# Optimization experiments

Hardware: AMD Instinct MI355X
Metric: run time of the kernel (lower is better)

## Reference

```python
import jax, jax.numpy as jnp
import numpy as np

HIDDEN_DIM = 2048
NUM_HEADS = 16
HEAD_DIM = HIDDEN_DIM // NUM_HEADS


def setup_inputs() -> dict:
    key = jax.random.key(0)
    ks = jax.random.split(key, 5)
    B, S, D = 1, 4096, HIDDEN_DIM
    scale = 1.0 / np.sqrt(D)
    x = jax.random.normal(ks[0], (B, S, D), dtype=jnp.float32)
    w_q = jax.random.normal(ks[1], (D, D), dtype=jnp.float32) * scale
    w_k = jax.random.normal(ks[2], (D, D), dtype=jnp.float32) * scale
    w_v = jax.random.normal(ks[3], (D, D), dtype=jnp.float32) * scale
    w_o = jax.random.normal(ks[4], (D, D), dtype=jnp.float32) * scale
    return {"x": x, "w_q": w_q, "w_k": w_k, "w_v": w_v, "w_o": w_o, "causal": 1}


def reference(x, w_q, w_k, w_v, w_o, causal):
    B, S, D = x.shape
    H, Dh = NUM_HEADS, HEAD_DIM
    sm_scale = 1.0 / np.sqrt(Dh)

    # projections (x @ W.T)
    q = jnp.einsum('bsd,ed->bse', x, w_q).reshape(B, S, H, Dh).transpose(0, 2, 1, 3)
    k = jnp.einsum('bsd,ed->bse', x, w_k).reshape(B, S, H, Dh).transpose(0, 2, 1, 3)
    v = jnp.einsum('bsd,ed->bse', x, w_v).reshape(B, S, H, Dh).transpose(0, 2, 1, 3)

    # attention scores [B, H, S, S]; flash online-softmax == standard softmax
    scores = jnp.einsum('bhqd,bhkd->bhqk', q, k) * sm_scale
    if causal:
        qpos = jnp.arange(S)[:, None]
        kpos = jnp.arange(S)[None, :]
        scores = jnp.where(qpos >= kpos, scores, -jnp.inf)
    probs = jax.nn.softmax(scores, axis=-1)
    o = jnp.einsum('bhqk,bhkd->bhqd', probs, v)  # [B, H, S, Dh]
    o = o.transpose(0, 2, 1, 3).reshape(B, S, D)
    return jnp.einsum('bsd,ed->bse', o, w_o)
```

## Files before the change

### kernel.cpp

```cpp
#include <hip/hip_runtime.h>
#include <stdint.h>

typedef __bf16 bf16_t;
typedef __bf16 bf16x8 __attribute__((ext_vector_type(8)));
typedef __bf16 bf16x4 __attribute__((ext_vector_type(4)));
typedef float  f32x4  __attribute__((ext_vector_type(4)));

static constexpr int S  = 4096;
static constexpr int D  = 2048;
static constexpr int H  = 16;
static constexpr int DH = 128;

__device__ __forceinline__ bf16x8 ld8(const bf16_t* p) { return *(const bf16x8*)p; }
__device__ __forceinline__ bf16x8 ld8c(const float* p) {
  const f32x4 a = *(const f32x4*)p;
  const f32x4 b = *(const f32x4*)(p + 4);
  bf16x8 r;
  r[0] = (bf16_t)a[0]; r[1] = (bf16_t)a[1]; r[2] = (bf16_t)a[2]; r[3] = (bf16_t)a[3];
  r[4] = (bf16_t)b[0]; r[5] = (bf16_t)b[1]; r[6] = (bf16_t)b[2]; r[7] = (bf16_t)b[3];
  return r;
}

__device__ __forceinline__ void async_ld16(const bf16_t* g, bf16_t* lds) {
  __builtin_amdgcn_global_load_lds(
      (const __attribute__((address_space(1))) uint32_t*)g,
      (__attribute__((address_space(3))) uint32_t*)lds, 16, 0, 0);
}

__global__ __launch_bounds__(256) void cvt_kernel(
    const float* __restrict__ x,  const float* __restrict__ wq,
    const float* __restrict__ wk, const float* __restrict__ wv,
    const float* __restrict__ wo,
    bf16_t* __restrict__ xb,  bf16_t* __restrict__ wqb,
    bf16_t* __restrict__ wkb, bf16_t* __restrict__ wvb,
    bf16_t* __restrict__ wob) {
  const int z = blockIdx.z;
  const float* src; bf16_t* dst; size_t off = 0;
  if      (z == 0) { src = x;  dst = xb;  off = 0; }
  else if (z == 1) { src = x;  dst = xb;  off = 4194304; }
  else if (z == 2) { src = wq; dst = wqb; }
  else if (z == 3) { src = wk; dst = wkb; }
  else if (z == 4) { src = wv; dst = wvb; }
  else             { src = wo; dst = wob; }
  const size_t i = off + ((size_t)blockIdx.x * 256 + threadIdx.x) * 8;
  *(bf16x8*)(dst + i) = ld8c(src + i);
}

template <typename TC, bool TR>
__device__ __forceinline__ void gemm_async(const bf16_t* __restrict__ A,
                                           const bf16_t* __restrict__ W,
                                           TC* __restrict__ C) {
  constexpr int K  = D;
  constexpr int BK = 32;
  __shared__ __align__(16) bf16_t Ash[128 * BK];
  __shared__ __align__(16) bf16_t Bsh[128 * BK];
  const int tid = threadIdx.x;
  const int w = tid >> 6, lane = tid & 63;
  const int c = lane & 15, g = lane >> 4;
  const int wm = w >> 1, wn = w & 1;
  const int rowBase = blockIdx.y * 128;
  const int colBase = blockIdx.x * 128;

  f32x4 acc[4][4] = {};

  for (int k0 = 0; k0 < K; k0 += BK) {
    __syncthreads();
    #pragma unroll
    for (int r = 0; r < 2; ++r) {
      const int cid = r * 256 + tid;
      const int row = cid >> 2, q = cid & 3;
      async_ld16(A + (size_t)(rowBase + row) * K + k0 + q * 8,
                 Ash + r * 2048 + w * 512);
      async_ld16(W + (size_t)(colBase + row) * K + k0 + q * 8,
                 Bsh + r * 2048 + w * 512);
    }
    __syncthreads();

    bf16x8 af[4], bf[4];
    #pragma unroll
    for (int i = 0; i < 4; ++i) af[i] = ld8(Ash + (wm * 64 + i * 16 + c) * BK + g * 8);
    #pragma unroll
    for (int j = 0; j < 4; ++j) bf[j] = ld8(Bsh + (wn * 64 + j * 16 + c) * BK + g * 8);
    #pragma unroll
    for (int i = 0; i < 4; ++i)
      #pragma unroll
      for (int j = 0; j < 4; ++j)
        acc[i][j] = __builtin_amdgcn_mfma_f32_16x16x32_bf16(af[i], bf[j], acc[i][j], 0, 0, 0);
  }

  #pragma unroll
  for (int i = 0; i < 4; ++i)
    #pragma unroll
    for (int j = 0; j < 4; ++j) {
      if (TR) {
        const int col  = colBase + wn * 64 + j * 16 + c;
        const int row0 = rowBase + wm * 64 + i * 16 + g * 4;
        bf16x4 v;
        #pragma unroll
        for (int r = 0; r < 4; ++r) v[r] = (bf16_t)acc[i][j][r];
        *(bf16x4*)((bf16_t*)C + (size_t)col * S + row0) = v;
      } else {
        #pragma unroll
        for (int r = 0; r < 4; ++r) {
          const int row = rowBase + wm * 64 + i * 16 + g * 4 + r;
          const int col = colBase + wn * 64 + j * 16 + c;
          C[(size_t)row * D + col] = (TC)acc[i][j][r];
        }
      }
    }
}

__global__ __launch_bounds__(256) void qkv_gemm_bf16(
    const bf16_t* __restrict__ X,
    const bf16_t* __restrict__ Wq, const bf16_t* __restrict__ Wk,
    const bf16_t* __restrict__ Wv,
    bf16_t* __restrict__ Qo, bf16_t* __restrict__ Ko, bf16_t* __restrict__ VTo) {
  if (blockIdx.z == 0)      gemm_async<bf16_t, false>(X, Wq, Qo);
  else if (blockIdx.z == 1) gemm_async<bf16_t, false>(X, Wk, Ko);
  else                      gemm_async<bf16_t, true >(X, Wv, VTo);
}

__global__ __launch_bounds__(256) void out_gemm_bf16(
    const bf16_t* __restrict__ A, const bf16_t* __restrict__ W,
    float* __restrict__ C) {
  gemm_async<float, false>(A, W, C);
}

__global__ __launch_bounds__(512, 2) void attn_kernel(
    const bf16_t* __restrict__ Q, const bf16_t* __restrict__ Kb,
    const bf16_t* __restrict__ VTg, bf16_t* __restrict__ O,
    const int* __restrict__ causal_p) {
  __shared__ __align__(16) bf16_t smem[40960];
  bf16_t* const KB0 = smem;
  bf16_t* const VB0 = smem + 16384;
  bf16_t* const Psh = smem + 32768;

  const int tid = threadIdx.x, w = tid >> 6, lane = tid & 63;
  const int c = lane & 15, g = lane >> 4;
  const int wq = w >> 1, wk = w & 1;
  const int causal = causal_p[0];
  constexpr float QS = 0.08838834764831845f * 1.4426950408889634f;

  const int bx = blockIdx.x;
  const int jj = bx >> 4;
  const int t = causal ? ((jj < 16) ? (31 - jj) : (jj - 16)) : jj;
  const int h = bx & 15;
  const int wrow = t * 128 + wq * 32;
  const int ktiles = causal ? (2 * t + 2) : (S / 64);

  int knA[2], qK8[2], dVA[2], qV8[2];
  #pragma unroll
  for (int r = 0; r < 2; ++r) {
    const int cid = r * 512 + tid;
    knA[r] = cid >> 4; qK8[r] = (((cid & 15) ^ (knA[r] & 7)) << 3);
    dVA[r] = cid >> 3; qV8[r] = (((cid & 7) ^ (dVA[r] & 7)) << 3);
  }

  bf16_t* const Pw = Psh + w * 1024;

  bf16x8 qf[2][4];
  #pragma unroll
  for (int i = 0; i < 2; ++i)
    #pragma unroll
    for (int kf = 0; kf < 4; ++kf) {
      const bf16x8 raw = ld8(Q + (size_t)(wrow + i * 16 + c) * D + h * DH + kf * 32 + g * 8);
      bf16x8 sc;
      #pragma unroll
      for (int e = 0; e < 8; ++e) sc[e] = (bf16_t)((float)raw[e] * QS);
      qf[i][kf] = sc;
    }

  f32x4 o_acc[2][8] = {};
  f32x4 psum[2] = {};

  #pragma unroll
  for (int r = 0; r < 2; ++r) {
    async_ld16(Kb + (size_t)knA[r] * D + h * DH + qK8[r], KB0 + r * 4096 + w * 512);
    async_ld16(VTg + (size_t)(h * DH + dVA[r]) * S + qV8[r], VB0 + r * 4096 + w * 512);
  }
  __syncthreads();

  int cur = 0;
  for (int kt = 0; kt < ktiles; ++kt) {
    if (kt + 1 < ktiles) {
      const int alt = cur ^ 1;
      #pragma unroll
      for (int r = 0; r < 2; ++r) {
        async_ld16(Kb + (size_t)((kt + 1) * 64 + knA[r]) * D + h * DH + qK8[r],
                   KB0 + alt * 8192 + r * 4096 + w * 512);
        async_ld16(VTg + (size_t)(h * DH + dVA[r]) * S + (kt + 1) * 64 + qV8[r],
                   VB0 + alt * 8192 + r * 4096 + w * 512);
      }
    }

    const bf16_t* const KB = KB0 + cur * 8192;
    const bf16_t* const VB = VB0 + cur * 8192;

    const bool active = !causal || (kt * 64 + wk * 32 <= wrow + 31);
    if (active) {
      __builtin_amdgcn_s_setprio(1);
      #pragma unroll
      for (int nf = 0; nf < 2; ++nf) {
        const int rr = wk * 32 + nf * 16 + c;
        f32x4 s[2] = {};
        #pragma unroll
        for (int kf = 0; kf < 4; ++kf) {
          const bf16x8 kk = ld8(KB + rr * 128 + ((((kf << 2) + g) ^ (rr & 7)) << 3));
          s[0] = __builtin_amdgcn_mfma_f32_16x16x32_bf16(qf[0][kf], kk, s[0], 0, 0, 0);
          s[1] = __builtin_amdgcn_mfma_f32_16x16x32_bf16(qf[1][kf], kk, s[1], 0, 0, 0);
        }
        if (causal && (kt * 64 + wk * 32 + nf * 16 + 15 > wrow)) {
          #pragma unroll
          for (int i = 0; i < 2; ++i)
            #pragma unroll
            for (int r_ = 0; r_ < 4; ++r_) {
              const int kc2 = kt * 64 + wk * 32 + nf * 16 + c;
              const int qr = wrow + i * 16 + g * 4 + r_;
              if (kc2 > qr) s[i][r_] = -1e30f;
            }
        }
        #pragma unroll
        for (int i = 0; i < 2; ++i)
          #pragma unroll
          for (int r_ = 0; r_ < 4; ++r_) {
            const int qrl = i * 16 + g * 4 + r_;
            const float pv = exp2f(s[i][r_]);
            psum[i][r_] += pv;
            const int ch = (((nf << 1) + (c >> 3)) + (qrl >> 1)) & 3;
            Pw[qrl * 32 + (ch << 3) + (c & 7)] = (bf16_t)pv;
          }
      }

      bf16x8 pf[2];
      #pragma unroll
      for (int i = 0; i < 2; ++i) {
        const int rowp = i * 16 + c;
        pf[i] = ld8(Pw + rowp * 32 + (((g + (rowp >> 1)) & 3) << 3));
      }
      #pragma unroll
      for (int nf = 0; nf < 8; ++nf) {
        const int dl = nf * 16 + c;
        const bf16x8 vf = ld8(VB + dl * 64 + ((((wk << 2) + g) ^ (dl & 7)) << 3));
        o_acc[0][nf] = __builtin_amdgcn_mfma_f32_16x16x32_bf16(pf[0], vf, o_acc[0][nf], 0, 0, 0);
        o_acc[1][nf] = __builtin_amdgcn_mfma_f32_16x16x32_bf16(pf[1], vf, o_acc[1][nf], 0, 0, 0);
      }
      __builtin_amdgcn_s_setprio(0);
    }

    __syncthreads();
    cur ^= 1;
  }

  float* const scr = (float*)smem;
  float* const slot = scr + (size_t)(wq * 64 + lane) * 72;
  if (wk == 1) {
    #pragma unroll
    for (int i = 0; i < 2; ++i) {
      #pragma unroll
      for (int nf = 0; nf < 8; ++nf)
        *(f32x4*)(slot + (i * 8 + nf) * 4) = o_acc[i][nf];
      *(f32x4*)(slot + 64 + i * 4) = psum[i];
    }
  }
  __syncthreads();
  if (wk == 0) {
    #pragma unroll
    for (int i = 0; i < 2; ++i) {
      #pragma unroll
      for (int nf = 0; nf < 8; ++nf)
        o_acc[i][nf] += *(const f32x4*)(slot + (i * 8 + nf) * 4);
      psum[i] += *(const f32x4*)(slot + 64 + i * 4);
    }
    #pragma unroll
    for (int i = 0; i < 2; ++i)
      #pragma unroll
      for (int r_ = 0; r_ < 4; ++r_) {
        float v = psum[i][r_];
        v += __shfl_xor(v, 1); v += __shfl_xor(v, 2);
        v += __shfl_xor(v, 4); v += __shfl_xor(v, 8);
        const float inv = 1.0f / v;
        const int row = wrow + i * 16 + g * 4 + r_;
        #pragma unroll
        for (int nf = 0; nf < 8; ++nf)
          O[(size_t)row * D + h * DH + nf * 16 + c] = (bf16_t)(o_acc[i][nf][r_] * inv);
      }
  }
}

extern "C" void kernel_launch(void* const* d_in, const int* in_sizes, int n_in,
                              void* d_out, int out_size, void* d_ws, size_t ws_size,
                              hipStream_t stream) {
  const float* x  = (const float*)d_in[0];
  const float* wq = (const float*)d_in[1];
  const float* wk = (const float*)d_in[2];
  const float* wv = (const float*)d_in[3];
  const float* wo = (const float*)d_in[4];
  const int* causal = (const int*)d_in[5];
  float* out = (float*)d_out;

  bf16_t* Qb  = (bf16_t*)d_ws;
  bf16_t* Kb  = Qb + (size_t)S * D;
  bf16_t* VTb = Kb + (size_t)S * D;
  bf16_t* Ob  = VTb + (size_t)S * D;
  bf16_t* xb  = Ob + (size_t)S * D;
  bf16_t* wqb = xb + (size_t)S * D;
  bf16_t* wkb = wqb + (size_t)D * D;
  bf16_t* wvb = wkb + (size_t)D * D;
  bf16_t* wob = wvb + (size_t)D * D;

  dim3 blk(256);
  cvt_kernel<<<dim3(2048, 1, 6), blk, 0, stream>>>(x, wq, wk, wv, wo,
                                                   xb, wqb, wkb, wvb, wob);
  qkv_gemm_bf16<<<dim3(D / 128, S / 128, 3), blk, 0, stream>>>(xb, wqb, wkb, wvb,
                                                               Qb, Kb, VTb);
  attn_kernel<<<dim3(512), dim3(512), 0, stream>>>(Qb, Kb, VTb, Ob, causal);
  out_gemm_bf16<<<dim3(D / 128, S / 128), blk, 0, stream>>>(Ob, wob, out);
}
```

Before: 442.6 us.

## Use persistent attention blocks with atomic work queue over 64-row query tiles

The attention kernel becomes persistent. Each block takes work items (head, 64-row query tile) from a global atomic counter, ordered longest-first under causal masking, instead of one fixed 128-row tile per block. Each wave now covers 16 query rows, computes S transposed (K as the A operand), and writes P as packed bf16x4 into a smaller LDS buffer. The aim is better load balance across CUs under the causal triangle. The cost is twice as many K/V tile loads per query row and an extra memset plus atomic synchronisation per item.

```diff
diff --git a/kernel.cpp b/kernel.cpp
--- a/kernel.cpp
+++ b/kernel.cpp
@@ -129,24 +129,18 @@
 __global__ __launch_bounds__(512, 2) void attn_kernel(
     const bf16_t* __restrict__ Q, const bf16_t* __restrict__ Kb,
     const bf16_t* __restrict__ VTg, bf16_t* __restrict__ O,
-    const int* __restrict__ causal_p) {
-  __shared__ __align__(16) bf16_t smem[40960];
+    const int* __restrict__ causal_p, int* __restrict__ ctr) {
+  __shared__ __align__(16) bf16_t smem[36864];
   bf16_t* const KB0 = smem;
   bf16_t* const VB0 = smem + 16384;
   bf16_t* const Psh = smem + 32768;
+  __shared__ int item_s;
 
   const int tid = threadIdx.x, w = tid >> 6, lane = tid & 63;
   const int c = lane & 15, g = lane >> 4;
   const int wq = w >> 1, wk = w & 1;
   const int causal = causal_p[0];
   constexpr float QS = 0.08838834764831845f * 1.4426950408889634f;
-
-  const int bx = blockIdx.x;
-  const int jj = bx >> 4;
-  const int t = causal ? ((jj < 16) ? (31 - jj) : (jj - 16)) : jj;
-  const int h = bx & 15;
-  const int wrow = t * 128 + wq * 32;
-  const int ktiles = causal ? (2 * t + 2) : (S / 64);
 
   int knA[2], qK8[2], dVA[2], qV8[2];
   #pragma unroll
@@ -156,134 +150,122 @@
     dVA[r] = cid >> 3; qV8[r] = (((cid & 7) ^ (dVA[r] & 7)) << 3);
   }
 
-  bf16_t* const Pw = Psh + w * 1024;
-
-  bf16x8 qf[2][4];
-  #pragma unroll
-  for (int i = 0; i < 2; ++i)
+  bf16_t* const Pw = Psh + w * 512;
+  const int psw = (c >> 1) & 3;
+
+  while (true) {
+    __syncthreads();
+    if (tid == 0) item_s = atomicAdd(ctr, 1);
+    __syncthreads();
+    const int it = item_s;
+    if (it >= 1024) break;
+    const int s64 = causal ? (63 - (it >> 4)) : (it >> 4);
+    const int h = it & 15;
+    const int qrow0 = s64 * 64 + wq * 16;
+    const int ktiles = causal ? (s64 + 1) : (S / 64);
+
+    bf16x8 qf[4];
     #pragma unroll
     for (int kf = 0; kf < 4; ++kf) {
-      const bf16x8 raw = ld8(Q + (size_t)(wrow + i * 16 + c) * D + h * DH + kf * 32 + g * 8);
+      const bf16x8 raw = ld8(Q + (size_t)(qrow0 + c) * D + h * DH + kf * 32 + g * 8);
       bf16x8 sc;
       #pragma unroll
       for (int e = 0; e < 8; ++e) sc[e] = (bf16_t)((float)raw[e] * QS);
-      qf[i][kf] = sc;
-    }
-
-  f32x4 o_acc[2][8] = {};
-  f32x4 psum[2] = {};
-
-  #pragma unroll
-  for (int r = 0; r < 2; ++r) {
-    async_ld16(Kb + (size_t)knA[r] * D + h * DH + qK8[r], KB0 + r * 4096 + w * 512);
-    async_ld16(VTg + (size_t)(h * DH + dVA[r]) * S + qV8[r], VB0 + r * 4096 + w * 512);
-  }
-  __syncthreads();
-
-  int cur = 0;
-  for (int kt = 0; kt < ktiles; ++kt) {
-    if (kt + 1 < ktiles) {
-      const int alt = cur ^ 1;
-      #pragma unroll
-      for (int r = 0; r < 2; ++r) {
-        async_ld16(Kb + (size_t)((kt + 1) * 64 + knA[r]) * D + h * DH + qK8[r],
-                   KB0 + alt * 8192 + r * 4096 + w * 512);
-        async_ld16(VTg + (size_t)(h * DH + dVA[r]) * S + (kt + 1) * 64 + qV8[r],
-                   VB0 + alt * 8192 + r * 4096 + w * 512);
+      qf[kf] = sc;
+    }
+
+    f32x4 o_acc[8] = {};
+    float psum = 0.0f;
+
+    #pragma unroll
+    for (int r = 0; r < 2; ++r) {
+      async_ld16(Kb + (size_t)knA[r] * D + h * DH + qK8[r], KB0 + r * 4096 + w * 512);
+      async_ld16(VTg + (size_t)(h * DH + dVA[r]) * S + qV8[r], VB0 + r * 4096 + w * 512);
+    }
+    __syncthreads();
+
+    int cur = 0;
+    for (int kt = 0; kt < ktiles; ++kt) {
+      if (kt + 1 < ktiles) {
+        const int alt = cur ^ 1;
+        #pragma unroll
+        for (int r = 0; r < 2; ++r) {
+          async_ld16(Kb + (size_t)((kt + 1) * 64 + knA[r]) * D + h * DH + qK8[r],
+                     KB0 + alt * 8192 + r * 4096 + w * 512);
+          async_ld16(VTg + (size_t)(h * DH + dVA[r]) * S + (kt + 1) * 64 + qV8[r],
+                     VB0 + alt * 8192 + r * 4096 + w * 512);
+        }
       }
-    }
-
-    const bf16_t* const KB = KB0 + cur * 8192;
-    const bf16_t* const VB = VB0 + cur * 8192;
-
-    const bool active = !causal || (kt * 64 + wk * 32 <= wrow + 31);
-    if (active) {
-      __builtin_amdgcn_s_setprio(1);
-      #pragma unroll
-      for (int nf = 0; nf < 2; ++nf) {
-        const int rr = wk * 32 + nf * 16 + c;
-        f32x4 s[2] = {};
-        #pragma unroll
-        for (int kf = 0; kf < 4; ++kf) {
-          const bf16x8 kk = ld8(KB + rr * 128 + ((((kf << 2) + g) ^ (rr & 7)) << 3));
-          s[0] = __builtin_amdgcn_mfma_f32_16x16x32_bf16(qf[0][kf], kk, s[0], 0, 0, 0);
-          s[1] = __builtin_amdgcn_mfma_f32_16x16x32_bf16(qf[1][kf], kk, s[1], 0, 0, 0);
-        }
-        if (causal && (kt * 64 + wk * 32 + nf * 16 + 15 > wrow)) {
+
+      const bf16_t* const KB = KB0 + cur * 8192;
+      const bf16_t* const VB = VB0 + cur * 8192;
+      const int kb = kt * 64 + wk * 32;
+
+      const bool active = !causal || (kb <= qrow0 + 15);
+      if (active) {
+        __builtin_amdgcn_s_setprio(1);
+        #pragma unroll
+        for (int nf = 0; nf < 2; ++nf) {
+          const int rr = wk * 32 + nf * 16 + c;
+          f32x4 s = {};
           #pragma unroll
-          for (int i = 0; i < 2; ++i)
+          for (int kf = 0; kf < 4; ++kf) {
+            const bf16x8 kk = ld8(KB + rr * 128 + ((((kf << 2) + g) ^ (rr & 7)) << 3));
+            s = __builtin_amdgcn_mfma_f32_16x16x32_bf16(kk, qf[kf], s, 0, 0, 0);
+          }
+          if (causal && (kb + nf * 16 + 15 > qrow0)) {
             #pragma unroll
-            for (int r_ = 0; r_ < 4; ++r_) {
-              const int kc2 = kt * 64 + wk * 32 + nf * 16 + c;
-              const int qr = wrow + i * 16 + g * 4 + r_;
-              if (kc2 > qr) s[i][r_] = -1e30f;
-            }
-        }
-        #pragma unroll
-        for (int i = 0; i < 2; ++i)
+            for (int r_ = 0; r_ < 4; ++r_)
+              if (kb + nf * 16 + g * 4 + r_ > qrow0 + c) s[r_] = -1e30f;
+          }
+          bf16x4 pq;
           #pragma unroll
           for (int r_ = 0; r_ < 4; ++r_) {
-            const int qrl = i * 16 + g * 4 + r_;
-            const float pv = exp2f(s[i][r_]);
-            psum[i][r_] += pv;
-            const int ch = (((nf << 1) + (c >> 3)) + (qrl >> 1)) & 3;
-            Pw[qrl * 32 + (ch << 3) + (c & 7)] = (bf16_t)pv;
+            const float pv = exp2f(s[r_]);
+            psum += pv;
+            pq[r_] = (bf16_t)pv;
           }
+          const int p  = (nf << 1) | (g >> 1);
+          const int pp = ((p ^ psw) << 1) | (g & 1);
+          *(bf16x4*)(Pw + c * 32 + pp * 4) = pq;
+        }
+
+        const bf16x8 pf = ld8(Pw + c * 32 + ((g ^ psw) << 3));
+        #pragma unroll
+        for (int nf = 0; nf < 8; ++nf) {
+          const int dl = nf * 16 + c;
+          const bf16x8 vf = ld8(VB + dl * 64 + ((((wk << 2) + g) ^ (dl & 7)) << 3));
+          o_acc[nf] = __builtin_amdgcn_mfma_f32_16x16x32_bf16(pf, vf, o_acc[nf], 0, 0, 0);
+        }
+        __builtin_amdgcn_s_setprio(0);
       }
 
-      bf16x8 pf[2];
-      #pragma unroll
-      for (int i = 0; i < 2; ++i) {
-        const int rowp = i * 16 + c;
-        pf[i] = ld8(Pw + rowp * 32 + (((g + (rowp >> 1)) & 3) << 3));
+      __syncthreads();
+      cur ^= 1;
+    }
+
+    float* const slot = (float*)smem + (size_t)(wq * 64 + lane) * 36;
+    if (wk == 1) {
+      #pragma unroll
+      for (int nf = 0; nf < 8; ++nf) *(f32x4*)(slot + nf * 4) = o_acc[nf];
+      slot[32] = psum;
+    }
+    __syncthreads();
+    if (wk == 0) {
+      #pragma unroll
+      for (int nf = 0; nf < 8; ++nf) o_acc[nf] += *(const f32x4*)(slot + nf * 4);
+      psum += slot[32];
+      float v = psum;
+      v += __shfl_xor(v, 16); v += __shfl_xor(v, 32);
+      #pragma unroll
+      for (int r_ = 0; r_ < 4; ++r_) {
+        const float inv = 1.0f / __shfl(v, g * 4 + r_, 64);
+        const int row = qrow0 + g * 4 + r_;
+        #pragma unroll
+        for (int nf = 0; nf < 8; ++nf)
+          O[(size_t)row * D + h * DH + nf * 16 + c] = (bf16_t)(o_acc[nf][r_] * inv);
       }
-      #pragma unroll
-      for (int nf = 0; nf < 8; ++nf) {
-        const int dl = nf * 16 + c;
-        const bf16x8 vf = ld8(VB + dl * 64 + ((((wk << 2) + g) ^ (dl & 7)) << 3));
-        o_acc[0][nf] = __builtin_amdgcn_mfma_f32_16x16x32_bf16(pf[0], vf, o_acc[0][nf], 0, 0, 0);
-        o_acc[1][nf] = __builtin_amdgcn_mfma_f32_16x16x32_bf16(pf[1], vf, o_acc[1][nf], 0, 0, 0);
-      }
-      __builtin_amdgcn_s_setprio(0);
-    }
-
-    __syncthreads();
-    cur ^= 1;
-  }
-
-  float* const scr = (float*)smem;
-  float* const slot = scr + (size_t)(wq * 64 + lane) * 72;
-  if (wk == 1) {
-    #pragma unroll
-    for (int i = 0; i < 2; ++i) {
-      #pragma unroll
-      for (int nf = 0; nf < 8; ++nf)
-        *(f32x4*)(slot + (i * 8 + nf) * 4) = o_acc[i][nf];
-      *(f32x4*)(slot + 64 + i * 4) = psum[i];
-    }
-  }
-  __syncthreads();
-  if (wk == 0) {
-    #pragma unroll
-    for (int i = 0; i < 2; ++i) {
-      #pragma unroll
-      for (int nf = 0; nf < 8; ++nf)
-        o_acc[i][nf] += *(const f32x4*)(slot + (i * 8 + nf) * 4);
-      psum[i] += *(const f32x4*)(slot + 64 + i * 4);
-    }
-    #pragma unroll
-    for (int i = 0; i < 2; ++i)
-      #pragma unroll
-      for (int r_ = 0; r_ < 4; ++r_) {
-        float v = psum[i][r_];
-        v += __shfl_xor(v, 1); v += __shfl_xor(v, 2);
-        v += __shfl_xor(v, 4); v += __shfl_xor(v, 8);
-        const float inv = 1.0f / v;
-        const int row = wrow + i * 16 + g * 4 + r_;
-        #pragma unroll
-        for (int nf = 0; nf < 8; ++nf)
-          O[(size_t)row * D + h * DH + nf * 16 + c] = (bf16_t)(o_acc[i][nf][r_] * inv);
-      }
+    }
   }
 }
 
@@ -307,12 +289,15 @@
   bf16_t* wkb = wqb + (size_t)D * D;
   bf16_t* wvb = wkb + (size_t)D * D;
   bf16_t* wob = wvb + (size_t)D * D;
+  int*    ctr = (int*)(wob + (size_t)D * D);
+
+  hipMemsetAsync(ctr, 0, sizeof(int), stream);
 
   dim3 blk(256);
   cvt_kernel<<<dim3(2048, 1, 6), blk, 0, stream>>>(x, wq, wk, wv, wo,
                                                    xb, wqb, wkb, wvb, wob);
   qkv_gemm_bf16<<<dim3(D / 128, S / 128, 3), blk, 0, stream>>>(xb, wqb, wkb, wvb,
                                                                Qb, Kb, VTb);
-  attn_kernel<<<dim3(512), dim3(512), 0, stream>>>(Qb, Kb, VTb, Ob, causal);
+  attn_kernel<<<dim3(512), dim3(512), 0, stream>>>(Qb, Kb, VTb, Ob, causal, ctr);
   out_gemm_bf16<<<dim3(D / 128, S / 128), blk, 0, stream>>>(Ob, wob, out);
 }
```

New measurement: 428.8 us. 1.03x faster.

## Make attention kernel persistent with atomic work queue in longest-first order

Applied to the files above, without the earlier changes.

The attention kernel becomes persistent: 384 workgroups repeatedly take (q-tile, head) items from a global atomic counter, ordered longest causal tile first, replacing the fixed 512-block grid with its paired ordering. It also swaps the QK^T MFMA operand order so each lane holds a query column, which lets P be written as packed bf16x4 stores and shrinks the row-sum to a scalar per lane reduced with fewer shuffles. The goal is to cut the load-imbalance tail from causal work and reduce LDS store traffic. It adds a memset and an atomic per item plus extra barriers, and the counter lives past the previous workspace end, which assumes the workspace has room for it.

```diff
diff --git a/kernel.cpp b/kernel.cpp
--- a/kernel.cpp
+++ b/kernel.cpp
@@ -129,24 +129,18 @@
 __global__ __launch_bounds__(512, 2) void attn_kernel(
     const bf16_t* __restrict__ Q, const bf16_t* __restrict__ Kb,
     const bf16_t* __restrict__ VTg, bf16_t* __restrict__ O,
-    const int* __restrict__ causal_p) {
+    const int* __restrict__ causal_p, int* __restrict__ ctr) {
   __shared__ __align__(16) bf16_t smem[40960];
   bf16_t* const KB0 = smem;
   bf16_t* const VB0 = smem + 16384;
   bf16_t* const Psh = smem + 32768;
+  __shared__ int item_s;
 
   const int tid = threadIdx.x, w = tid >> 6, lane = tid & 63;
   const int c = lane & 15, g = lane >> 4;
   const int wq = w >> 1, wk = w & 1;
   const int causal = causal_p[0];
   constexpr float QS = 0.08838834764831845f * 1.4426950408889634f;
-
-  const int bx = blockIdx.x;
-  const int jj = bx >> 4;
-  const int t = causal ? ((jj < 16) ? (31 - jj) : (jj - 16)) : jj;
-  const int h = bx & 15;
-  const int wrow = t * 128 + wq * 32;
-  const int ktiles = causal ? (2 * t + 2) : (S / 64);
 
   int knA[2], qK8[2], dVA[2], qV8[2];
   #pragma unroll
@@ -157,133 +151,152 @@
   }
 
   bf16_t* const Pw = Psh + w * 1024;
-
-  bf16x8 qf[2][4];
-  #pragma unroll
-  for (int i = 0; i < 2; ++i)
-    #pragma unroll
-    for (int kf = 0; kf < 4; ++kf) {
-      const bf16x8 raw = ld8(Q + (size_t)(wrow + i * 16 + c) * D + h * DH + kf * 32 + g * 8);
-      bf16x8 sc;
-      #pragma unroll
-      for (int e = 0; e < 8; ++e) sc[e] = (bf16_t)((float)raw[e] * QS);
-      qf[i][kf] = sc;
-    }
-
-  f32x4 o_acc[2][8] = {};
-  f32x4 psum[2] = {};
-
-  #pragma unroll
-  for (int r = 0; r < 2; ++r) {
-    async_ld16(Kb + (size_t)knA[r] * D + h * DH + qK8[r], KB0 + r * 4096 + w * 512);
-    async_ld16(VTg + (size_t)(h * DH + dVA[r]) * S + qV8[r], VB0 + r * 4096 + w * 512);
-  }
-  __syncthreads();
-
-  int cur = 0;
-  for (int kt = 0; kt < ktiles; ++kt) {
-    if (kt + 1 < ktiles) {
-      const int alt = cur ^ 1;
-      #pragma unroll
-      for (int r = 0; r < 2; ++r) {
-        async_ld16(Kb + (size_t)((kt + 1) * 64 + knA[r]) * D + h * DH + qK8[r],
-                   KB0 + alt * 8192 + r * 4096 + w * 512);
-        async_ld16(VTg + (size_t)(h * DH + dVA[r]) * S + (kt + 1) * 64 + qV8[r],
-                   VB0 + alt * 8192 + r * 4096 + w * 512);
-      }
-    }
-
-    const bf16_t* const KB = KB0 + cur * 8192;
-    const bf16_t* const VB = VB0 + cur * 8192;
-
-    const bool active = !causal || (kt * 64 + wk * 32 <= wrow + 31);
-    if (active) {
-      __builtin_amdgcn_s_setprio(1);
-      #pragma unroll
-      for (int nf = 0; nf < 2; ++nf) {
-        const int rr = wk * 32 + nf * 16 + c;
-        f32x4 s[2] = {};
-        #pragma unroll
-        for (int kf = 0; kf < 4; ++kf) {
-          const bf16x8 kk = ld8(KB + rr * 128 + ((((kf << 2) + g) ^ (rr & 7)) << 3));
-          s[0] = __builtin_amdgcn_mfma_f32_16x16x32_bf16(qf[0][kf], kk, s[0], 0, 0, 0);
-          s[1] = __builtin_amdgcn_mfma_f32_16x16x32_bf16(qf[1][kf], kk, s[1], 0, 0, 0);
-        }
-        if (causal && (kt * 64 + wk * 32 + nf * 16 + 15 > wrow)) {
+  const int psw = (c >> 1) & 3;
+
+  while (true) {
+    if (tid == 0) item_s = atomicAdd(ctr, 1);
+    __syncthreads();
+    const int it = item_s;
+    if (it >= 512) break;
+    const int t = causal ? (31 - (it >> 4)) : (it >> 4);
+    const int h = it & 15;
+    const int qrow0 = t * 128 + wq * 32;
+    const int ktiles = causal ? (2 * t + 2) : (S / 64);
+
+    const bf16_t* kSrc[2];
+    const bf16_t* vSrc[2];
+    #pragma unroll
+    for (int r = 0; r < 2; ++r) {
+      kSrc[r] = Kb + (size_t)knA[r] * D + h * DH + qK8[r];
+      vSrc[r] = VTg + (size_t)(h * DH + dVA[r]) * S + qV8[r];
+    }
+    #pragma unroll
+    for (int r = 0; r < 2; ++r) {
+      async_ld16(kSrc[r], KB0 + r * 4096 + w * 512);
+      async_ld16(vSrc[r], VB0 + r * 4096 + w * 512);
+      kSrc[r] += (size_t)64 * D;
+      vSrc[r] += 64;
+    }
+
+    bf16x8 qf[2][4];
+    #pragma unroll
+    for (int i = 0; i < 2; ++i)
+      #pragma unroll
+      for (int kf = 0; kf < 4; ++kf) {
+        const bf16x8 raw = ld8(Q + (size_t)(qrow0 + i * 16 + c) * D + h * DH + kf * 32 + g * 8);
+        bf16x8 sc;
+        #pragma unroll
+        for (int e = 0; e < 8; ++e) sc[e] = (bf16_t)((float)raw[e] * QS);
+        qf[i][kf] = sc;
+      }
+
+    f32x4 o_acc[2][8] = {};
+    float psum[2] = {0.0f, 0.0f};
+
+    __syncthreads();
+
+    int cur = 0;
+    for (int kt = 0; kt < ktiles; ++kt) {
+      if (kt + 1 < ktiles) {
+        const int alt = cur ^ 1;
+        #pragma unroll
+        for (int r = 0; r < 2; ++r) {
+          async_ld16(kSrc[r], KB0 + alt * 8192 + r * 4096 + w * 512);
+          async_ld16(vSrc[r], VB0 + alt * 8192 + r * 4096 + w * 512);
+          kSrc[r] += (size_t)64 * D;
+          vSrc[r] += 64;
+        }
+      }
+
+      const bf16_t* const KB = KB0 + cur * 8192;
+      const bf16_t* const VB = VB0 + cur * 8192;
+      const int kb = kt * 64 + wk * 32;
+
+      const bool active = !causal || (kb <= qrow0 + 31);
+      if (active) {
+        __builtin_amdgcn_s_setprio(1);
+        #pragma unroll
+        for (int nf = 0; nf < 2; ++nf) {
+          const int rr = wk * 32 + nf * 16 + c;
+          bf16x8 kk[4];
           #pragma unroll
-          for (int i = 0; i < 2; ++i)
+          for (int kf = 0; kf < 4; ++kf)
+            kk[kf] = ld8(KB + rr * 128 + ((((kf << 2) + g) ^ (rr & 7)) << 3));
+          #pragma unroll
+          for (int i = 0; i < 2; ++i) {
+            f32x4 s = {};
+            #pragma unroll
+            for (int kf = 0; kf < 4; ++kf)
+              s = __builtin_amdgcn_mfma_f32_16x16x32_bf16(kk[kf], qf[i][kf], s, 0, 0, 0);
+            if (causal && (kb + nf * 16 + 15 > qrow0 + i * 16)) {
+              #pragma unroll
+              for (int r_ = 0; r_ < 4; ++r_)
+                if (kb + nf * 16 + g * 4 + r_ > qrow0 + i * 16 + c) s[r_] = -1e30f;
+            }
+            bf16x4 pq;
             #pragma unroll
             for (int r_ = 0; r_ < 4; ++r_) {
-              const int kc2 = kt * 64 + wk * 32 + nf * 16 + c;
-              const int qr = wrow + i * 16 + g * 4 + r_;
-              if (kc2 > qr) s[i][r_] = -1e30f;
+              const float pv = exp2f(s[r_]);
+              psum[i] += pv;
+              pq[r_] = (bf16_t)pv;
             }
-        }
+            const int p  = (nf << 1) | (g >> 1);
+            const int pp = ((p ^ psw) << 1) | (g & 1);
+            *(bf16x4*)(Pw + i * 512 + c * 32 + pp * 4) = pq;
+          }
+        }
+
+        bf16x8 pf[2];
         #pragma unroll
         for (int i = 0; i < 2; ++i)
+          pf[i] = ld8(Pw + i * 512 + c * 32 + ((g ^ psw) << 3));
+        #pragma unroll
+        for (int nf = 0; nf < 8; ++nf) {
+          const int dl = nf * 16 + c;
+          const bf16x8 vf = ld8(VB + dl * 64 + ((((wk << 2) + g) ^ (dl & 7)) << 3));
+          o_acc[0][nf] = __builtin_amdgcn_mfma_f32_16x16x32_bf16(pf[0], vf, o_acc[0][nf], 0, 0, 0);
+          o_acc[1][nf] = __builtin_amdgcn_mfma_f32_16x16x32_bf16(pf[1], vf, o_acc[1][nf], 0, 0, 0);
+        }
+        __builtin_amdgcn_s_setprio(0);
+      }
+
+      __syncthreads();
+      cur ^= 1;
+    }
+
+    float* const slot = (float*)smem + (size_t)(wq * 64 + lane) * 72;
+    if (wk == 1) {
+      #pragma unroll
+      for (int i = 0; i < 2; ++i)
+        #pragma unroll
+        for (int nf = 0; nf < 8; ++nf)
+          *(f32x4*)(slot + (i * 8 + nf) * 4) = o_acc[i][nf];
+      slot[64] = psum[0];
+      slot[65] = psum[1];
+    }
+    __syncthreads();
+    if (wk == 0) {
+      #pragma unroll
+      for (int i = 0; i < 2; ++i)
+        #pragma unroll
+        for (int nf = 0; nf < 8; ++nf)
+          o_acc[i][nf] += *(const f32x4*)(slot + (i * 8 + nf) * 4);
+      psum[0] += slot[64];
+      psum[1] += slot[65];
+      #pragma unroll
+      for (int i = 0; i < 2; ++i) {
+        float v = psum[i];
+        v += __shfl_xor(v, 16); v += __shfl_xor(v, 32);
+        #pragma unroll
+        for (int r_ = 0; r_ < 4; ++r_) {
+          const float inv = 1.0f / __shfl(v, g * 4 + r_, 64);
+          const int row = qrow0 + i * 16 + g * 4 + r_;
           #pragma unroll
-          for (int r_ = 0; r_ < 4; ++r_) {
-            const int qrl = i * 16 + g * 4 + r_;
-            const float pv = exp2f(s[i][r_]);
-            psum[i][r_] += pv;
-            const int ch = (((nf << 1) + (c >> 3)) + (qrl >> 1)) & 3;
-            Pw[qrl * 32 + (ch << 3) + (c & 7)] = (bf16_t)pv;
-          }
-      }
-
-      bf16x8 pf[2];
-      #pragma unroll
-      for (int i = 0; i < 2; ++i) {
-        const int rowp = i * 16 + c;
-        pf[i] = ld8(Pw + rowp * 32 + (((g + (rowp >> 1)) & 3) << 3));
-      }
-      #pragma unroll
-      for (int nf = 0; nf < 8; ++nf) {
-        const int dl = nf * 16 + c;
-        const bf16x8 vf = ld8(VB + dl * 64 + ((((wk << 2) + g) ^ (dl & 7)) << 3));
-        o_acc[0][nf] = __builtin_amdgcn_mfma_f32_16x16x32_bf16(pf[0], vf, o_acc[0][nf], 0, 0, 0);
-        o_acc[1][nf] = __builtin_amdgcn_mfma_f32_16x16x32_bf16(pf[1], vf, o_acc[1][nf], 0, 0, 0);
-      }
-      __builtin_amdgcn_s_setprio(0);
-    }
-
-    __syncthreads();
-    cur ^= 1;
-  }
-
-  float* const scr = (float*)smem;
-  float* const slot = scr + (size_t)(wq * 64 + lane) * 72;
-  if (wk == 1) {
-    #pragma unroll
-    for (int i = 0; i < 2; ++i) {
-      #pragma unroll
-      for (int nf = 0; nf < 8; ++nf)
-        *(f32x4*)(slot + (i * 8 + nf) * 4) = o_acc[i][nf];
-      *(f32x4*)(slot + 64 + i * 4) = psum[i];
-    }
-  }
-  __syncthreads();
-  if (wk == 0) {
-    #pragma unroll
-    for (int i = 0; i < 2; ++i) {
-      #pragma unroll
-      for (int nf = 0; nf < 8; ++nf)
-        o_acc[i][nf] += *(const f32x4*)(slot + (i * 8 + nf) * 4);
-      psum[i] += *(const f32x4*)(slot + 64 + i * 4);
-    }
-    #pragma unroll
-    for (int i = 0; i < 2; ++i)
-      #pragma unroll
-      for (int r_ = 0; r_ < 4; ++r_) {
-        float v = psum[i][r_];
-        v += __shfl_xor(v, 1); v += __shfl_xor(v, 2);
-        v += __shfl_xor(v, 4); v += __shfl_xor(v, 8);
-        const float inv = 1.0f / v;
-        const int row = wrow + i * 16 + g * 4 + r_;
-        #pragma unroll
-        for (int nf = 0; nf < 8; ++nf)
-          O[(size_t)row * D + h * DH + nf * 16 + c] = (bf16_t)(o_acc[i][nf][r_] * inv);
-      }
+          for (int nf = 0; nf < 8; ++nf)
+            O[(size_t)row * D + h * DH + nf * 16 + c] = (bf16_t)(o_acc[i][nf][r_] * inv);
+        }
+      }
+    }
   }
 }
 
@@ -307,12 +320,15 @@
   bf16_t* wkb = wqb + (size_t)D * D;
   bf16_t* wvb = wkb + (size_t)D * D;
   bf16_t* wob = wvb + (size_t)D * D;
+  int*    ctr = (int*)(wob + (size_t)D * D);
+
+  hipMemsetAsync(ctr, 0, sizeof(int), stream);
 
   dim3 blk(256);
   cvt_kernel<<<dim3(2048, 1, 6), blk, 0, stream>>>(x, wq, wk, wv, wo,
                                                    xb, wqb, wkb, wvb, wob);
   qkv_gemm_bf16<<<dim3(D / 128, S / 128, 3), blk, 0, stream>>>(xb, wqb, wkb, wvb,
                                                                Qb, Kb, VTb);
-  attn_kernel<<<dim3(512), dim3(512), 0, stream>>>(Qb, Kb, VTb, Ob, causal);
+  attn_kernel<<<dim3(384), dim3(512), 0, stream>>>(Qb, Kb, VTb, Ob, causal, ctr);
   out_gemm_bf16<<<dim3(D / 128, S / 128), blk, 0, stream>>>(Ob, wob, out);
 }
```

Result: no change. 437.4 us (-1.2%).
